# Optimization experiments

Measured on AMD Instinct MI355X. Metric: run time of the kernel, lower is better.

The kernel has to match this reference:

```python
import jax, jax.numpy as jnp
import numpy as np

B, D, H, E, TOPK, NTASK = 16384, 128, 4, 8, 2, 1
ODIM = D // H  # MoE expert output dim (input_feat // num_heads)


def setup_inputs() -> dict:
    key = jax.random.key(0)
    ks = jax.random.split(key, 12)
    s = lambda k, shp, fan: jax.random.normal(k, shp, jnp.float32) / np.sqrt(fan)
    return {
        "x": jax.random.normal(ks[0], (B, D), jnp.float32),
        "Wq": s(ks[1], (D, D * H), D), "bq": jnp.zeros((D * H,), jnp.float32),
        "Wk": s(ks[2], (D, D * H), D), "bk": jnp.zeros((D * H,), jnp.float32),
        "Wg": s(ks[3], (D, E), D),
        "W1": s(ks[4], (E, D, D), D), "b1": jnp.zeros((E, D), jnp.float32),
        "W2": s(ks[5], (E, D, ODIM), D), "b2": jnp.zeros((E, ODIM), jnp.float32),
        "Wout": s(ks[6], (H * ODIM, NTASK), H * ODIM),
        "bout": jnp.zeros((NTASK,), jnp.float32),
    }


def reference(x, Wq, bq, Wk, bk, Wg, W1, b1, W2, b2, Wout, bout):
    # query/key projections -> [B, H, D] token views, flattened to [N, D]
    tok = (x @ Wq + bq).reshape(B * H, D)
    gate_tok = (x @ Wk + bk).reshape(B * H, D)

    # gating: softmax over experts, top-2 routing with renormalized weights
    probs = jax.nn.softmax(gate_tok @ Wg, axis=-1)          # [N, E]
    top_p, top_i = jax.lax.top_k(probs, TOPK)               # [N, k]
    weights = top_p / jnp.sum(top_p, axis=-1, keepdims=True)

    # expert MLPs (dense all-expert compute, then gather selected)
    h = jax.nn.relu(jnp.einsum('nd,edh->neh', tok, W1) + b1)  # [N, E, D]
    eo = jnp.einsum('neh,eho->neo', h, W2) + b2               # [N, E, ODIM]
    sel = jnp.take_along_axis(eo, top_i[:, :, None], axis=1)  # [N, k, ODIM]
    y = jnp.sum(weights[:, :, None] * sel, axis=1)            # [N, ODIM]

    # load-balancing auxiliary loss (switch-style): E * sum(frac_i * mean_prob_i)
    one_hot = jax.nn.one_hot(top_i[:, 0], E, dtype=probs.dtype)
    frac = jnp.mean(one_hot, axis=0)
    mean_p = jnp.mean(probs, axis=0)
    aux_loss = E * jnp.sum(frac * mean_p)

    out = y.reshape(B, H * ODIM) @ Wout + bout                # [B, NTASK]
    return out, aux_loss
```

## Files before the change

kernel.cpp:

```cpp
#include <hip/hip_runtime.h>
#include <hip/hip_bf16.h>

#define BB   16384
#define DD   128
#define HH   4
#define EE   8
#define NN   (BB*HH)
#define OD   32
#define PT   136
#define CAP  24576

typedef __attribute__((ext_vector_type(8))) short short8;
typedef __attribute__((ext_vector_type(4))) short short4v;
typedef __attribute__((ext_vector_type(4))) float f32x4;

static __device__ __forceinline__ short f2bf(float v) {
    unsigned int u = __builtin_bit_cast(unsigned int, v);
    u = (u + 0x7FFFu + ((u >> 16) & 1u)) >> 16;
    return (short)u;
}

__global__ __launch_bounds__(256) void prep(
    const float* __restrict__ Wq, const float* __restrict__ Wk, const float* __restrict__ Wg,
    const float* __restrict__ bk, const float* __restrict__ W1, const float* __restrict__ W2,
    const float* __restrict__ bout,
    short* __restrict__ WqF, short* __restrict__ W1F, short* __restrict__ W2F,
    float* __restrict__ Wkg, float* __restrict__ bkg, float* __restrict__ out,
    int* __restrict__ cursors)
{
    int idx = blockIdx.x * 256 + threadIdx.x;
    if (idx < 65536) {
        int j = idx & 7, lane = (idx >> 3) & 63, ks = (idx >> 9) & 3, ct = idx >> 11;
        int l16 = lane & 15, quad = lane >> 4;
        int c = ct * 16 + l16, k = ks * 32 + quad * 8 + j;
        WqF[idx] = f2bf(Wq[k * 512 + c]);
    } else if (idx < 196608) {
        int r = idx - 65536;
        int j = r & 7, lane = (r >> 3) & 63, ks = (r >> 9) & 3, mt = (r >> 11) & 7, e = r >> 14;
        int l16 = lane & 15, quad = lane >> 4;
        int m = mt * 16 + l16, k = ks * 32 + quad * 8 + j;
        W1F[r] = f2bf(W1[e * 16384 + k * 128 + m]);
    } else if (idx < 229376) {
        int r = idx - 196608;
        int j = r & 7, lane = (r >> 3) & 63, ks = (r >> 9) & 3, mt = (r >> 11) & 1, e = r >> 12;
        int l16 = lane & 15, quad = lane >> 4;
        int m = mt * 16 + l16, k = ks * 32 + quad * 8 + j;
        W2F[r] = f2bf(W2[e * 4096 + k * 32 + m]);
    } else if (idx < 233472) {
        int r = idx - 229376;
        int k = r >> 5, col = r & 31, hh = col >> 3, e = col & 7;
        float s = 0.f;
        #pragma unroll 8
        for (int d = 0; d < 128; ++d) s += Wk[k * 512 + hh * 128 + d] * Wg[d * 8 + e];
        Wkg[k * 32 + col] = s;
    } else if (idx < 233504) {
        int r = idx - 233472;
        int hh = r >> 3, e = r & 7;
        float s = 0.f;
        #pragma unroll 8
        for (int d = 0; d < 128; ++d) s += bk[hh * 128 + d] * Wg[d * 8 + e];
        bkg[r] = s;
    } else if (idx < 249888) {
        out[idx - 233504] = bout[0];
    } else if (idx < 249896) {
        int r = idx - 249888;
        cursors[r] = r * CAP;
    }
}

__global__ __launch_bounds__(256) void k1_fused(
    const float* __restrict__ x, const short* __restrict__ WqF, const float* __restrict__ bq,
    const float* __restrict__ Wkg, const float* __restrict__ bkg,
    short* __restrict__ tokb, float* __restrict__ wts, float* __restrict__ blkPart,
    int* __restrict__ cursors, int* __restrict__ listIdx)
{
    __shared__ __align__(16) char smem[64 * 129 * 4];
    __shared__ float lps[EE];
    __shared__ float lcn[EE];
    __shared__ int   lcnt[EE];
    __shared__ int   lbase[EE];

    const int t = threadIdx.x;

    if (blockIdx.x < 512) {
        short* xL = (short*)smem;
        const int b0 = blockIdx.x * 32;

        {
            int slot = t >> 3, seg = t & 7;
            const float4* src = (const float4*)(x + (size_t)(b0 + slot) * 128 + seg * 16);
            float4 v0 = src[0], v1 = src[1], v2 = src[2], v3 = src[3];
            short8 a, b;
            a[0]=f2bf(v0.x); a[1]=f2bf(v0.y); a[2]=f2bf(v0.z); a[3]=f2bf(v0.w);
            a[4]=f2bf(v1.x); a[5]=f2bf(v1.y); a[6]=f2bf(v1.z); a[7]=f2bf(v1.w);
            b[0]=f2bf(v2.x); b[1]=f2bf(v2.y); b[2]=f2bf(v2.z); b[3]=f2bf(v2.w);
            b[4]=f2bf(v3.x); b[5]=f2bf(v3.y); b[6]=f2bf(v3.z); b[7]=f2bf(v3.w);
            *(short8*)(xL + slot * PT + seg * 16)     = a;
            *(short8*)(xL + slot * PT + seg * 16 + 8) = b;
        }
        __syncthreads();

        const int wv   = t >> 6;
        const int lane = t & 63;
        const int l16  = lane & 15;
        const int quad = lane >> 4;

        f32x4 acc[8][2];
        #pragma unroll
        for (int ml = 0; ml < 8; ++ml)
            #pragma unroll
            for (int nl = 0; nl < 2; ++nl)
                acc[ml][nl] = (f32x4){0.f, 0.f, 0.f, 0.f};

        short8 bf[2][4];
        #pragma unroll
        for (int nl = 0; nl < 2; ++nl)
            #pragma unroll
            for (int ks = 0; ks < 4; ++ks)
                bf[nl][ks] = *(const short8*)(xL + (nl*16 + l16) * PT + ks*32 + quad*8);

        #pragma unroll
        for (int ks = 0; ks < 4; ++ks) {
            short8 af[8];
            #pragma unroll
            for (int ml = 0; ml < 8; ++ml)
                af[ml] = *(const short8*)(WqF + ((size_t)(((wv*8 + ml)*4 + ks)*64 + lane)) * 8);
            #pragma unroll
            for (int ml = 0; ml < 8; ++ml)
                #pragma unroll
                for (int nl = 0; nl < 2; ++nl)
                    acc[ml][nl] = __builtin_amdgcn_mfma_f32_16x16x32_bf16(af[ml], bf[nl][ks], acc[ml][nl], 0, 0, 0);
        }

        #pragma unroll
        for (int ml = 0; ml < 8; ++ml) {
            int c0 = wv*128 + ml*16 + quad*4;
            f32x4 bqv = *(const f32x4*)(bq + c0);
            #pragma unroll
            for (int nl = 0; nl < 2; ++nl) {
                int b = b0 + nl*16 + l16;
                short4v hv;
                #pragma unroll
                for (int r = 0; r < 4; ++r) hv[r] = f2bf(acc[ml][nl][r] + bqv[r]);
                *(short4v*)(tokb + (size_t)b * 512 + c0) = hv;
            }
        }
        return;
    }

    float* xG = (float*)smem;
    const int gb = blockIdx.x - 512;
    const int b0 = gb * 64;

    if (t < EE) { lps[t] = 0.f; lcn[t] = 0.f; lcnt[t] = 0; }

    for (int i = t; i < 2048; i += 256) {
        int r = i >> 5, c = i & 31;
        float4 v = ((const float4*)(x + (size_t)(b0 + r) * 128))[c];
        float* dst = xG + r * 129 + c * 4;
        dst[0] = v.x; dst[1] = v.y; dst[2] = v.z; dst[3] = v.w;
    }
    __syncthreads();

    const int h  = __builtin_amdgcn_readfirstlane(t >> 6);
    const int lb = t & 63;

    const f32x4* wkg4 = (const f32x4*)Wkg;
    f32x4 a0 = ((const f32x4*)bkg)[h * 2];
    f32x4 a1 = ((const f32x4*)bkg)[h * 2 + 1];

    const float* xrow = xG + lb * 129;
    #pragma unroll 4
    for (int k = 0; k < 128; ++k) {
        float xv = xrow[k];
        f32x4 w0 = wkg4[k * 8 + h * 2];
        f32x4 w1 = wkg4[k * 8 + h * 2 + 1];
        a0 += w0 * xv;
        a1 += w1 * xv;
    }

    float l[8] = {a0[0], a0[1], a0[2], a0[3], a1[0], a1[1], a1[2], a1[3]};
    float mx = l[0];
    #pragma unroll
    for (int e = 1; e < 8; ++e) mx = fmaxf(mx, l[e]);
    float p[8]; float sm = 0.f;
    #pragma unroll
    for (int e = 0; e < 8; ++e) { p[e] = __expf(l[e] - mx); sm += p[e]; }
    float isin = 1.f / sm;
    #pragma unroll
    for (int e = 0; e < 8; ++e) p[e] *= isin;

    int i1 = 0; float p1 = p[0];
    #pragma unroll
    for (int e = 1; e < 8; ++e) if (p[e] > p1) { p1 = p[e]; i1 = e; }
    int i2 = (i1 == 0) ? 1 : 0; float p2 = p[i2];
    #pragma unroll
    for (int e = 0; e < 8; ++e) if (e != i1 && p[e] > p2) { p2 = p[e]; i2 = e; }

    int n = (b0 + lb) * 4 + h;
    float rinv = 1.f / (p1 + p2);
    wts[2*n]    = p1 * rinv; wts[2*n+1]  = p2 * rinv;

    int s0 = atomicAdd(&lcnt[i1], 1);
    int s1 = atomicAdd(&lcnt[i2], 1);

    #pragma unroll
    for (int e = 0; e < 8; ++e) {
        float v = p[e];
        #pragma unroll
        for (int m2 = 1; m2 < 64; m2 <<= 1) v += __shfl_xor(v, m2);
        unsigned long long m1b = __ballot(i1 == e);
        if (lb == 0) {
            atomicAdd(&lps[e], v);
            atomicAdd(&lcn[e], (float)__popcll(m1b));
        }
    }
    __syncthreads();
    if (t < EE) lbase[t] = atomicAdd(&cursors[t], lcnt[t]);
    __syncthreads();

    int q0 = lbase[i1] + s0;
    if (q0 < (i1 + 1) * CAP) listIdx[q0] = 2*n;
    int q1 = lbase[i2] + s1;
    if (q1 < (i2 + 1) * CAP) listIdx[q1] = 2*n + 1;

    if (t < EE) {
        float* bp = blkPart + gb * 16;
        bp[t]     = lps[t];
        bp[8 + t] = lcn[t];
    }
}

__global__ __launch_bounds__(256) void k2b_expert(
    const short* __restrict__ tokb, const short* __restrict__ W1F,
    const float* __restrict__ b1, const short* __restrict__ W2F, const float* __restrict__ b2,
    const int* __restrict__ cursors, const int* __restrict__ listIdx,
    const float* __restrict__ wts, const float* __restrict__ Wout,
    const float* __restrict__ blkPart, float* __restrict__ out)
{
    __shared__ short tokL[64 * PT];
    __shared__ short hL[64 * PT];
    __shared__ int   ids[64];
    __shared__ float wsl[64];
    __shared__ float WoutL[128];
    __shared__ float red[16][16];
    __shared__ float fin[16];

    const int e = blockIdx.y;
    const int t = threadIdx.x;

    if (blockIdx.x == gridDim.x - 1 && e == 7) {
        int chunk = t >> 4, col = t & 15;
        float v = 0.f;
        for (int i = 0; i < 16; ++i) v += blkPart[(chunk * 16 + i) * 16 + col];
        red[chunk][col] = v;
        __syncthreads();
        if (t < 16) {
            float s = 0.f;
            #pragma unroll
            for (int c = 0; c < 16; ++c) s += red[c][t];
            fin[t] = s;
        }
        __syncthreads();
        if (t == 0) {
            float aux = 0.f;
            const float invN = 1.f / (float)NN;
            for (int e2 = 0; e2 < EE; ++e2) aux += (fin[8 + e2] * invN) * (fin[e2] * invN);
            out[BB] = (float)EE * aux;
        }
    }

    int cnt = cursors[e] - e * CAP;
    if (cnt > CAP) cnt = CAP;
    const int off = blockIdx.x * 64;
    if (off >= cnt) return;
    const int sb  = e * CAP + off;
    const int nt  = min(64, cnt - off);

    if (t < 64) {
        int a = listIdx[sb + min(t, nt - 1)];
        ids[t] = a >> 1;
        wsl[t] = (t < nt) ? wts[a] : 0.f;
    }
    if (t >= 128 && t < 256) WoutL[t - 128] = Wout[t - 128];
    __syncthreads();

    #pragma unroll
    for (int r = 0; r < 4; ++r) {
        int i = t + r * 256;
        int slot = i >> 4, seg = i & 15;
        short8 v = *(const short8*)(tokb + (size_t)ids[slot] * 128 + seg * 8);
        *(short8*)(tokL + slot * PT + seg * 8) = v;
    }
    __syncthreads();

    const int wv   = t >> 6;
    const int lane = t & 63;
    const int l16  = lane & 15;
    const int quad = lane >> 4;

    f32x4 acc[2][4];
    #pragma unroll
    for (int ml = 0; ml < 2; ++ml)
        #pragma unroll
        for (int nl = 0; nl < 4; ++nl)
            acc[ml][nl] = (f32x4){0.f, 0.f, 0.f, 0.f};

    short8 af[2][4];
    #pragma unroll
    for (int ml = 0; ml < 2; ++ml)
        #pragma unroll
        for (int ks = 0; ks < 4; ++ks)
            af[ml][ks] = *(const short8*)(W1F + ((size_t)(((e*8 + wv*2 + ml)*4 + ks)*64 + lane)) * 8);

    short8 bf[4][4];
    #pragma unroll
    for (int nl = 0; nl < 4; ++nl)
        #pragma unroll
        for (int ks = 0; ks < 4; ++ks)
            bf[nl][ks] = *(const short8*)(tokL + (nl*16 + l16) * PT + ks*32 + quad*8);

    #pragma unroll
    for (int ks = 0; ks < 4; ++ks)
        #pragma unroll
        for (int ml = 0; ml < 2; ++ml)
            #pragma unroll
            for (int nl = 0; nl < 4; ++nl)
                acc[ml][nl] = __builtin_amdgcn_mfma_f32_16x16x32_bf16(af[ml][ks], bf[nl][ks], acc[ml][nl], 0, 0, 0);

    #pragma unroll
    for (int ml = 0; ml < 2; ++ml) {
        int hid0 = wv*32 + ml*16 + quad*4;
        f32x4 b1v = *(const f32x4*)(b1 + e*128 + hid0);
        #pragma unroll
        for (int nl = 0; nl < 4; ++nl) {
            short4v hv;
            #pragma unroll
            for (int r = 0; r < 4; ++r) {
                float v = acc[ml][nl][r] + b1v[r];
                hv[r] = f2bf(fmaxf(v, 0.f));
            }
            *(short4v*)(hL + (nl*16 + l16) * PT + hid0) = hv;
        }
    }
    __syncthreads();

    f32x4 acc2[2];
    acc2[0] = (f32x4){0.f, 0.f, 0.f, 0.f};
    acc2[1] = (f32x4){0.f, 0.f, 0.f, 0.f};

    short8 af2[2][4];
    #pragma unroll
    for (int ml = 0; ml < 2; ++ml)
        #pragma unroll
        for (int ks = 0; ks < 4; ++ks)
            af2[ml][ks] = *(const short8*)(W2F + ((size_t)(((e*2 + ml)*4 + ks)*64 + lane)) * 8);

    short8 bf2[4];
    #pragma unroll
    for (int ks = 0; ks < 4; ++ks)
        bf2[ks] = *(const short8*)(hL + (wv*16 + l16) * PT + ks*32 + quad*8);

    #pragma unroll
    for (int ks = 0; ks < 4; ++ks)
        #pragma unroll
        for (int ml = 0; ml < 2; ++ml)
            acc2[ml] = __builtin_amdgcn_mfma_f32_16x16x32_bf16(af2[ml][ks], bf2[ks], acc2[ml], 0, 0, 0);

    const int slot = wv*16 + l16;
    const int nn   = ids[slot];
    const int hsel = nn & 3;
    float partial = 0.f;
    #pragma unroll
    for (int ml = 0; ml < 2; ++ml) {
        int od0 = ml*16 + quad*4;
        f32x4 b2v = *(const f32x4*)(b2 + e*32 + od0);
        const float* wseg = WoutL + hsel*32 + od0;
        #pragma unroll
        for (int r = 0; r < 4; ++r)
            partial += (acc2[ml][r] + b2v[r]) * wseg[r];
    }
    partial += __shfl_xor(partial, 16);
    partial += __shfl_xor(partial, 32);
    if (quad == 0) {
        float v = partial * wsl[slot];
        atomicAdd(&out[nn >> 2], v);
    }
}

extern "C" void kernel_launch(void* const* d_in, const int* in_sizes, int n_in,
                              void* d_out, int out_size, void* d_ws, size_t ws_size,
                              hipStream_t stream) {
    (void)in_sizes; (void)n_in; (void)out_size; (void)ws_size;
    const float* x    = (const float*)d_in[0];
    const float* Wq   = (const float*)d_in[1];
    const float* bq   = (const float*)d_in[2];
    const float* Wk   = (const float*)d_in[3];
    const float* bk   = (const float*)d_in[4];
    const float* Wg   = (const float*)d_in[5];
    const float* W1   = (const float*)d_in[6];
    const float* b1   = (const float*)d_in[7];
    const float* W2   = (const float*)d_in[8];
    const float* b2   = (const float*)d_in[9];
    const float* Wout = (const float*)d_in[10];
    const float* bout = (const float*)d_in[11];
    float* out = (float*)d_out;

    char* ws = (char*)d_ws;
    short* tokb     = (short*)(ws + 0);
    float* wts      = (float*)(ws + 16777216);
    int*   listIdx  = (int*)  (ws + 17301504);
    short* WqF      = (short*)(ws + 18087936);
    short* W1F      = (short*)(ws + 18219008);
    short* W2F      = (short*)(ws + 18481152);
    float* Wkg      = (float*)(ws + 18546688);
    float* bkg      = (float*)(ws + 18563072);
    float* blkPart  = (float*)(ws + 18563200);
    int*   cursors  = (int*)  (ws + 18579584);

    prep<<<977, 256, 0, stream>>>(Wq, Wk, Wg, bk, W1, W2, bout, WqF, W1F, W2F, Wkg, bkg, out, cursors);
    k1_fused<<<768, 256, 0, stream>>>(x, WqF, bq, Wkg, bkg, tokb, wts, blkPart, cursors, listIdx);
    k2b_expert<<<dim3(CAP/64, 8), 256, 0, stream>>>(tokb, W1F, b1, W2F, b2, cursors, listIdx, wts, Wout, blkPart, out);
}
```

Before: 124.5 us.

## Fold Wq projection into per-head expert W1 weights and drop token materialization

Precomputes per-(expert,head) combined weights A1 = Wq_h·W1_e and bias1 = bq_h·W1_e + b1_e, so expert blocks read the bf16 input row x directly. This removes the large query-projection GEMM and the 16 MB bf16 token buffer write and read. Routing lists are now split into 32 (expert,head) buckets with smaller capacity. The cost is a small per-call weight-fusion GEMM, an extra bf16 rounding of the fused weights, and a risk of overflowing the smaller per-bucket capacity under skewed routing.

```diff
diff --git a/kernel.cpp b/kernel.cpp
--- a/kernel.cpp
+++ b/kernel.cpp
@@ -8,7 +8,8 @@
 #define NN   (BB*HH)
 #define OD   32
 #define PT   136
-#define CAP  24576
+#define NL   32
+#define CAP2 6144
 
 typedef __attribute__((ext_vector_type(8))) short short8;
 typedef __attribute__((ext_vector_type(4))) short short4v;
@@ -19,145 +20,166 @@
     u = (u + 0x7FFFu + ((u >> 16) & 1u)) >> 16;
     return (short)u;
 }
-
-__global__ __launch_bounds__(256) void prep(
-    const float* __restrict__ Wq, const float* __restrict__ Wk, const float* __restrict__ Wg,
-    const float* __restrict__ bk, const float* __restrict__ W1, const float* __restrict__ W2,
+static __device__ __forceinline__ float bf2f(short b) {
+    unsigned int u = ((unsigned int)(unsigned short)b) << 16;
+    return __builtin_bit_cast(float, u);
+}
+
+__global__ __launch_bounds__(256) void prep2(
+    const float* __restrict__ x, const float* __restrict__ Wq, const float* __restrict__ bq,
+    const float* __restrict__ Wk, const float* __restrict__ Wg, const float* __restrict__ bk,
+    const float* __restrict__ W1, const float* __restrict__ b1, const float* __restrict__ W2,
     const float* __restrict__ bout,
-    short* __restrict__ WqF, short* __restrict__ W1F, short* __restrict__ W2F,
-    float* __restrict__ Wkg, float* __restrict__ bkg, float* __restrict__ out,
-    int* __restrict__ cursors)
+    short* __restrict__ xb, short* __restrict__ A1F, float* __restrict__ bias1,
+    short* __restrict__ W2F, float* __restrict__ Wkg, float* __restrict__ bkg,
+    float* __restrict__ out, int* __restrict__ cursors)
 {
-    int idx = blockIdx.x * 256 + threadIdx.x;
-    if (idx < 65536) {
-        int j = idx & 7, lane = (idx >> 3) & 63, ks = (idx >> 9) & 3, ct = idx >> 11;
-        int l16 = lane & 15, quad = lane >> 4;
-        int c = ct * 16 + l16, k = ks * 32 + quad * 8 + j;
-        WqF[idx] = f2bf(Wq[k * 512 + c]);
-    } else if (idx < 196608) {
-        int r = idx - 65536;
-        int j = r & 7, lane = (r >> 3) & 63, ks = (r >> 9) & 3, mt = (r >> 11) & 7, e = r >> 14;
-        int l16 = lane & 15, quad = lane >> 4;
-        int m = mt * 16 + l16, k = ks * 32 + quad * 8 + j;
-        W1F[r] = f2bf(W1[e * 16384 + k * 128 + m]);
-    } else if (idx < 229376) {
-        int r = idx - 196608;
-        int j = r & 7, lane = (r >> 3) & 63, ks = (r >> 9) & 3, mt = (r >> 11) & 1, e = r >> 12;
-        int l16 = lane & 15, quad = lane >> 4;
-        int m = mt * 16 + l16, k = ks * 32 + quad * 8 + j;
-        W2F[r] = f2bf(W2[e * 4096 + k * 32 + m]);
-    } else if (idx < 233472) {
-        int r = idx - 229376;
-        int k = r >> 5, col = r & 31, hh = col >> 3, e = col & 7;
-        float s = 0.f;
-        #pragma unroll 8
-        for (int d = 0; d < 128; ++d) s += Wk[k * 512 + hh * 128 + d] * Wg[d * 8 + e];
-        Wkg[k * 32 + col] = s;
-    } else if (idx < 233504) {
-        int r = idx - 233472;
-        int hh = r >> 3, e = r & 7;
-        float s = 0.f;
-        #pragma unroll 8
-        for (int d = 0; d < 128; ++d) s += bk[hh * 128 + d] * Wg[d * 8 + e];
-        bkg[r] = s;
-    } else if (idx < 249888) {
-        out[idx - 233504] = bout[0];
-    } else if (idx < 249896) {
-        int r = idx - 249888;
-        cursors[r] = r * CAP;
-    }
-}
-
-__global__ __launch_bounds__(256) void k1_fused(
-    const float* __restrict__ x, const short* __restrict__ WqF, const float* __restrict__ bq,
-    const float* __restrict__ Wkg, const float* __restrict__ bkg,
-    short* __restrict__ tokb, float* __restrict__ wts, float* __restrict__ blkPart,
-    int* __restrict__ cursors, int* __restrict__ listIdx)
-{
-    __shared__ __align__(16) char smem[64 * 129 * 4];
-    __shared__ float lps[EE];
-    __shared__ float lcn[EE];
-    __shared__ int   lcnt[EE];
-    __shared__ int   lbase[EE];
-
-    const int t = threadIdx.x;
-
-    if (blockIdx.x < 512) {
-        short* xL = (short*)smem;
-        const int b0 = blockIdx.x * 32;
-
-        {
-            int slot = t >> 3, seg = t & 7;
-            const float4* src = (const float4*)(x + (size_t)(b0 + slot) * 128 + seg * 16);
+    if (blockIdx.x < 32) {
+        __shared__ short L[128 * PT];
+        const int li = blockIdx.x;
+        const int e = li >> 2, h = li & 3;
+        const int t = threadIdx.x;
+        const int wv = t >> 6, lane = t & 63, l16 = lane & 15, quad = lane >> 4;
+
+        #pragma unroll
+        for (int rep = 0; rep < 16; ++rep) {
+            int idx = t + rep * 256;
+            int c = idx >> 5, h4 = (idx & 31) * 4;
+            float4 v = *(const float4*)(W1 + e * 16384 + c * 128 + h4);
+            L[(h4 + 0) * PT + c] = f2bf(v.x);
+            L[(h4 + 1) * PT + c] = f2bf(v.y);
+            L[(h4 + 2) * PT + c] = f2bf(v.z);
+            L[(h4 + 3) * PT + c] = f2bf(v.w);
+        }
+        __syncthreads();
+
+        short8 af[2][4];
+        #pragma unroll
+        for (int ml = 0; ml < 2; ++ml)
+            #pragma unroll
+            for (int ks = 0; ks < 4; ++ks)
+                af[ml][ks] = *(const short8*)(L + ((wv*2 + ml)*16 + l16) * PT + ks*32 + quad*8);
+        if (t < 128) {
+            float s = 0.f;
+            #pragma unroll 8
+            for (int c = 0; c < 128; ++c)
+                s += bq[h*128 + c] * bf2f(L[t * PT + c]);
+            bias1[li*128 + t] = s + b1[e*128 + t];
+        }
+        __syncthreads();
+
+        #pragma unroll
+        for (int rep = 0; rep < 4; ++rep) {
+            int idx = t + rep * 256;
+            int d = idx >> 3, c0 = (idx & 7) * 16;
+            const float4* src = (const float4*)(Wq + d * 512 + h * 128 + c0);
             float4 v0 = src[0], v1 = src[1], v2 = src[2], v3 = src[3];
             short8 a, b;
             a[0]=f2bf(v0.x); a[1]=f2bf(v0.y); a[2]=f2bf(v0.z); a[3]=f2bf(v0.w);
             a[4]=f2bf(v1.x); a[5]=f2bf(v1.y); a[6]=f2bf(v1.z); a[7]=f2bf(v1.w);
             b[0]=f2bf(v2.x); b[1]=f2bf(v2.y); b[2]=f2bf(v2.z); b[3]=f2bf(v2.w);
             b[4]=f2bf(v3.x); b[5]=f2bf(v3.y); b[6]=f2bf(v3.z); b[7]=f2bf(v3.w);
-            *(short8*)(xL + slot * PT + seg * 16)     = a;
-            *(short8*)(xL + slot * PT + seg * 16 + 8) = b;
-        }
-        __syncthreads();
-
-        const int wv   = t >> 6;
-        const int lane = t & 63;
-        const int l16  = lane & 15;
-        const int quad = lane >> 4;
-
-        f32x4 acc[8][2];
-        #pragma unroll
-        for (int ml = 0; ml < 8; ++ml)
-            #pragma unroll
-            for (int nl = 0; nl < 2; ++nl)
-                acc[ml][nl] = (f32x4){0.f, 0.f, 0.f, 0.f};
-
-        short8 bf[2][4];
-        #pragma unroll
-        for (int nl = 0; nl < 2; ++nl)
-            #pragma unroll
-            for (int ks = 0; ks < 4; ++ks)
-                bf[nl][ks] = *(const short8*)(xL + (nl*16 + l16) * PT + ks*32 + quad*8);
-
+            *(short8*)(L + d * PT + c0)     = a;
+            *(short8*)(L + d * PT + c0 + 8) = b;
+        }
+        __syncthreads();
+
+        f32x4 acc[2][8];
+        #pragma unroll
+        for (int ml = 0; ml < 2; ++ml)
+            #pragma unroll
+            for (int nt = 0; nt < 8; ++nt)
+                acc[ml][nt] = (f32x4){0.f, 0.f, 0.f, 0.f};
         #pragma unroll
         for (int ks = 0; ks < 4; ++ks) {
-            short8 af[8];
-            #pragma unroll
-            for (int ml = 0; ml < 8; ++ml)
-                af[ml] = *(const short8*)(WqF + ((size_t)(((wv*8 + ml)*4 + ks)*64 + lane)) * 8);
-            #pragma unroll
-            for (int ml = 0; ml < 8; ++ml)
+            short8 bf[8];
+            #pragma unroll
+            for (int nt = 0; nt < 8; ++nt)
+                bf[nt] = *(const short8*)(L + (nt*16 + l16) * PT + ks*32 + quad*8);
+            #pragma unroll
+            for (int ml = 0; ml < 2; ++ml)
                 #pragma unroll
-                for (int nl = 0; nl < 2; ++nl)
-                    acc[ml][nl] = __builtin_amdgcn_mfma_f32_16x16x32_bf16(af[ml], bf[nl][ks], acc[ml][nl], 0, 0, 0);
-        }
-
-        #pragma unroll
-        for (int ml = 0; ml < 8; ++ml) {
-            int c0 = wv*128 + ml*16 + quad*4;
-            f32x4 bqv = *(const f32x4*)(bq + c0);
-            #pragma unroll
-            for (int nl = 0; nl < 2; ++nl) {
-                int b = b0 + nl*16 + l16;
-                short4v hv;
+                for (int nt = 0; nt < 8; ++nt)
+                    acc[ml][nt] = __builtin_amdgcn_mfma_f32_16x16x32_bf16(af[ml][ks], bf[nt], acc[ml][nt], 0, 0, 0);
+        }
+        __syncthreads();
+
+        #pragma unroll
+        for (int ml = 0; ml < 2; ++ml)
+            #pragma unroll
+            for (int nt = 0; nt < 8; ++nt)
                 #pragma unroll
-                for (int r = 0; r < 4; ++r) hv[r] = f2bf(acc[ml][nl][r] + bqv[r]);
-                *(short4v*)(tokb + (size_t)b * 512 + c0) = hv;
+                for (int r = 0; r < 4; ++r)
+                    L[((wv*2 + ml)*16 + quad*4 + r) * PT + nt*16 + l16] = f2bf(acc[ml][nt][r]);
+        __syncthreads();
+
+        #pragma unroll
+        for (int mt = 0; mt < 8; ++mt)
+            #pragma unroll
+            for (int ks = 0; ks < 4; ++ks) {
+                short8 v = *(const short8*)(L + (mt*16 + l16) * PT + ks*32 + quad*8);
+                *(short8*)(A1F + ((size_t)(((li*8 + mt)*4 + ks)*64 + lane)) * 8) = v;
             }
-        }
         return;
     }
 
-    float* xG = (float*)smem;
-    const int gb = blockIdx.x - 512;
-    const int b0 = gb * 64;
-
-    if (t < EE) { lps[t] = 0.f; lcn[t] = 0.f; lcnt[t] = 0; }
+    int idx = (blockIdx.x - 32) * 256 + threadIdx.x;
+    if (idx < 262144) {
+        const float4* x4 = (const float4*)x;
+        float4 v0 = x4[idx * 2], v1 = x4[idx * 2 + 1];
+        short8 s;
+        s[0]=f2bf(v0.x); s[1]=f2bf(v0.y); s[2]=f2bf(v0.z); s[3]=f2bf(v0.w);
+        s[4]=f2bf(v1.x); s[5]=f2bf(v1.y); s[6]=f2bf(v1.z); s[7]=f2bf(v1.w);
+        *(short8*)(xb + (size_t)idx * 8) = s;
+    } else if (idx < 294912) {
+        int r = idx - 262144;
+        int j = r & 7, lane = (r >> 3) & 63, ks = (r >> 9) & 3, mt = (r >> 11) & 1, e = r >> 12;
+        int l16 = lane & 15, quad = lane >> 4;
+        int m = mt * 16 + l16, k = ks * 32 + quad * 8 + j;
+        W2F[r] = f2bf(W2[e * 4096 + k * 32 + m]);
+    } else if (idx < 299008) {
+        int r = idx - 294912;
+        int k = r >> 5, col = r & 31, hh = col >> 3, e = col & 7;
+        float s = 0.f;
+        #pragma unroll 8
+        for (int d = 0; d < 128; ++d) s += Wk[k * 512 + hh * 128 + d] * Wg[d * 8 + e];
+        Wkg[k * 32 + col] = s;
+    } else if (idx < 299040) {
+        int r = idx - 299008;
+        int hh = r >> 3, e = r & 7;
+        float s = 0.f;
+        #pragma unroll 8
+        for (int d = 0; d < 128; ++d) s += bk[hh * 128 + d] * Wg[d * 8 + e];
+        bkg[r] = s;
+    } else if (idx < 315424) {
+        out[idx - 299040] = bout[0];
+    } else if (idx < 315456) {
+        int r = idx - 315424;
+        cursors[r] = r * CAP2;
+    }
+}
+
+__global__ __launch_bounds__(256) void k1_gate(
+    const float* __restrict__ x, const float* __restrict__ Wkg, const float* __restrict__ bkg,
+    float* __restrict__ wts, float* __restrict__ blkPart,
+    int* __restrict__ cursors, int* __restrict__ listIdx)
+{
+    __shared__ float xL[64 * 129];
+    __shared__ float lps[EE];
+    __shared__ float lcn[EE];
+    __shared__ int   lcnt[NL];
+    __shared__ int   lbase[NL];
+
+    const int t  = threadIdx.x;
+    const int b0 = blockIdx.x * 64;
+
+    if (t < EE) { lps[t] = 0.f; lcn[t] = 0.f; }
+    if (t < NL) lcnt[t] = 0;
 
     for (int i = t; i < 2048; i += 256) {
         int r = i >> 5, c = i & 31;
         float4 v = ((const float4*)(x + (size_t)(b0 + r) * 128))[c];
-        float* dst = xG + r * 129 + c * 4;
+        float* dst = xL + r * 129 + c * 4;
         dst[0] = v.x; dst[1] = v.y; dst[2] = v.z; dst[3] = v.w;
     }
     __syncthreads();
@@ -169,7 +191,7 @@
     f32x4 a0 = ((const f32x4*)bkg)[h * 2];
     f32x4 a1 = ((const f32x4*)bkg)[h * 2 + 1];
 
-    const float* xrow = xG + lb * 129;
+    const float* xrow = xL + lb * 129;
     #pragma unroll 4
     for (int k = 0; k < 128; ++k) {
         float xv = xrow[k];
@@ -201,8 +223,9 @@
     float rinv = 1.f / (p1 + p2);
     wts[2*n]    = p1 * rinv; wts[2*n+1]  = p2 * rinv;
 
-    int s0 = atomicAdd(&lcnt[i1], 1);
-    int s1 = atomicAdd(&lcnt[i2], 1);
+    int li0 = i1 * 4 + h, li1 = i2 * 4 + h;
+    int s0 = atomicAdd(&lcnt[li0], 1);
+    int s1 = atomicAdd(&lcnt[li1], 1);
 
     #pragma unroll
     for (int e = 0; e < 8; ++e) {
@@ -216,24 +239,24 @@
         }
     }
     __syncthreads();
-    if (t < EE) lbase[t] = atomicAdd(&cursors[t], lcnt[t]);
-    __syncthreads();
-
-    int q0 = lbase[i1] + s0;
-    if (q0 < (i1 + 1) * CAP) listIdx[q0] = 2*n;
-    int q1 = lbase[i2] + s1;
-    if (q1 < (i2 + 1) * CAP) listIdx[q1] = 2*n + 1;
+    if (t < NL) lbase[t] = atomicAdd(&cursors[t], lcnt[t]);
+    __syncthreads();
+
+    int q0 = lbase[li0] + s0;
+    if (q0 < (li0 + 1) * CAP2) listIdx[q0] = 2*n;
+    int q1 = lbase[li1] + s1;
+    if (q1 < (li1 + 1) * CAP2) listIdx[q1] = 2*n + 1;
 
     if (t < EE) {
-        float* bp = blkPart + gb * 16;
+        float* bp = blkPart + blockIdx.x * 16;
         bp[t]     = lps[t];
         bp[8 + t] = lcn[t];
     }
 }
 
 __global__ __launch_bounds__(256) void k2b_expert(
-    const short* __restrict__ tokb, const short* __restrict__ W1F,
-    const float* __restrict__ b1, const short* __restrict__ W2F, const float* __restrict__ b2,
+    const short* __restrict__ xb, const short* __restrict__ A1F,
+    const float* __restrict__ bias1, const short* __restrict__ W2F, const float* __restrict__ b2,
     const int* __restrict__ cursors, const int* __restrict__ listIdx,
     const float* __restrict__ wts, const float* __restrict__ Wout,
     const float* __restrict__ blkPart, float* __restrict__ out)
@@ -242,14 +265,15 @@
     __shared__ short hL[64 * PT];
     __shared__ int   ids[64];
     __shared__ float wsl[64];
-    __shared__ float WoutL[128];
     __shared__ float red[16][16];
     __shared__ float fin[16];
 
-    const int e = blockIdx.y;
-    const int t = threadIdx.x;
-
-    if (blockIdx.x == gridDim.x - 1 && e == 7) {
+    const int li = blockIdx.y;
+    const int e  = li >> 2;
+    const int h  = li & 3;
+    const int t  = threadIdx.x;
+
+    if (blockIdx.x == gridDim.x - 1 && li == NL - 1) {
         int chunk = t >> 4, col = t & 15;
         float v = 0.f;
         for (int i = 0; i < 16; ++i) v += blkPart[(chunk * 16 + i) * 16 + col];
@@ -270,26 +294,25 @@
         }
     }
 
-    int cnt = cursors[e] - e * CAP;
-    if (cnt > CAP) cnt = CAP;
+    int cnt = cursors[li] - li * CAP2;
+    if (cnt > CAP2) cnt = CAP2;
     const int off = blockIdx.x * 64;
     if (off >= cnt) return;
-    const int sb  = e * CAP + off;
+    const int sb  = li * CAP2 + off;
     const int nt  = min(64, cnt - off);
 
     if (t < 64) {
         int a = listIdx[sb + min(t, nt - 1)];
-        ids[t] = a >> 1;
+        ids[t] = a >> 3;
         wsl[t] = (t < nt) ? wts[a] : 0.f;
     }
-    if (t >= 128 && t < 256) WoutL[t - 128] = Wout[t - 128];
     __syncthreads();
 
     #pragma unroll
     for (int r = 0; r < 4; ++r) {
         int i = t + r * 256;
         int slot = i >> 4, seg = i & 15;
-        short8 v = *(const short8*)(tokb + (size_t)ids[slot] * 128 + seg * 8);
+        short8 v = *(const short8*)(xb + (size_t)ids[slot] * 128 + seg * 8);
         *(short8*)(tokL + slot * PT + seg * 8) = v;
     }
     __syncthreads();
@@ -311,7 +334,7 @@
     for (int ml = 0; ml < 2; ++ml)
         #pragma unroll
         for (int ks = 0; ks < 4; ++ks)
-            af[ml][ks] = *(const short8*)(W1F + ((size_t)(((e*8 + wv*2 + ml)*4 + ks)*64 + lane)) * 8);
+            af[ml][ks] = *(const short8*)(A1F + ((size_t)(((li*8 + wv*2 + ml)*4 + ks)*64 + lane)) * 8);
 
     short8 bf[4][4];
     #pragma unroll
@@ -331,7 +354,7 @@
     #pragma unroll
     for (int ml = 0; ml < 2; ++ml) {
         int hid0 = wv*32 + ml*16 + quad*4;
-        f32x4 b1v = *(const f32x4*)(b1 + e*128 + hid0);
+        f32x4 b1v = *(const f32x4*)(bias1 + li*128 + hid0);
         #pragma unroll
         for (int nl = 0; nl < 4; ++nl) {
             short4v hv;
@@ -368,23 +391,22 @@
             acc2[ml] = __builtin_amdgcn_mfma_f32_16x16x32_bf16(af2[ml][ks], bf2[ks], acc2[ml], 0, 0, 0);
 
     const int slot = wv*16 + l16;
-    const int nn   = ids[slot];
-    const int hsel = nn & 3;
+    const int b    = ids[slot];
     float partial = 0.f;
     #pragma unroll
     for (int ml = 0; ml < 2; ++ml) {
         int od0 = ml*16 + quad*4;
         f32x4 b2v = *(const f32x4*)(b2 + e*32 + od0);
-        const float* wseg = WoutL + hsel*32 + od0;
+        f32x4 wv4 = *(const f32x4*)(Wout + h*32 + od0);
         #pragma unroll
         for (int r = 0; r < 4; ++r)
-            partial += (acc2[ml][r] + b2v[r]) * wseg[r];
+            partial += (acc2[ml][r] + b2v[r]) * wv4[r];
     }
     partial += __shfl_xor(partial, 16);
     partial += __shfl_xor(partial, 32);
     if (quad == 0) {
         float v = partial * wsl[slot];
-        atomicAdd(&out[nn >> 2], v);
+        atomicAdd(&out[b], v);
     }
 }
 
@@ -407,18 +429,20 @@
     float* out = (float*)d_out;
 
     char* ws = (char*)d_ws;
-    short* tokb     = (short*)(ws + 0);
-    float* wts      = (float*)(ws + 16777216);
-    int*   listIdx  = (int*)  (ws + 17301504);
-    short* WqF      = (short*)(ws + 18087936);
-    short* W1F      = (short*)(ws + 18219008);
-    short* W2F      = (short*)(ws + 18481152);
-    float* Wkg      = (float*)(ws + 18546688);
-    float* bkg      = (float*)(ws + 18563072);
-    float* blkPart  = (float*)(ws + 18563200);
-    int*   cursors  = (int*)  (ws + 18579584);
-
-    prep<<<977, 256, 0, stream>>>(Wq, Wk, Wg, bk, W1, W2, bout, WqF, W1F, W2F, Wkg, bkg, out, cursors);
-    k1_fused<<<768, 256, 0, stream>>>(x, WqF, bq, Wkg, bkg, tokb, wts, blkPart, cursors, listIdx);
-    k2b_expert<<<dim3(CAP/64, 8), 256, 0, stream>>>(tokb, W1F, b1, W2F, b2, cursors, listIdx, wts, Wout, blkPart, out);
-}
+    short* xb       = (short*)(ws + 0);
+    float* wts      = (float*)(ws + 4194304);
+    int*   listIdx  = (int*)  (ws + 4718592);
+    short* A1F      = (short*)(ws + 5505024);
+    short* W2F      = (short*)(ws + 6553600);
+    float* Wkg      = (float*)(ws + 6619136);
+    float* bkg      = (float*)(ws + 6635520);
+    float* bias1    = (float*)(ws + 6635648);
+    float* blkPart  = (float*)(ws + 6652032);
+    int*   cursors  = (int*)  (ws + 6668416);
+
+    prep2<<<1265, 256, 0, stream>>>(x, Wq, bq, Wk, Wg, bk, W1, b1, W2, bout,
+                                    xb, A1F, bias1, W2F, Wkg, bkg, out, cursors);
+    k1_gate<<<256, 256, 0, stream>>>(x, Wkg, bkg, wts, blkPart, cursors, listIdx);
+    k2b_expert<<<dim3(CAP2/64, NL), 256, 0, stream>>>(xb, A1F, bias1, W2F, b2,
+                                    cursors, listIdx, wts, Wout, blkPart, out);
+}
```

Measured after the change: 131.9 us. +6.0%, slower.
